# Kernel tuning notes

Hardware: AMD Instinct MI355X
Metric: run time of the kernel (lower is better)

## Reference

```python
import jax, jax.numpy as jnp
import numpy as np

TEMP = 0.1
DX = 64  # feature dim of x; W1 rows [0:DX] multiply x, rows [DX:] multiply y


def setup_inputs() -> dict:
    key = jax.random.key(0)
    k1, k2, k3, k4 = jax.random.split(key, 4)
    n, d, hidden = 1024, 64, 256
    x = jax.random.normal(k1, (n, d), dtype=jnp.float32)
    y = jax.random.normal(k2, (n, d), dtype=jnp.float32)
    W1 = jax.random.normal(k3, (2 * d, hidden), dtype=jnp.float32) * (1.0 / np.sqrt(2 * d))
    b1 = jnp.zeros((hidden,), dtype=jnp.float32)
    w2 = jax.random.normal(k4, (hidden,), dtype=jnp.float32) * (1.0 / np.sqrt(hidden))
    b2 = jnp.zeros((), dtype=jnp.float32)
    return {"x": x, "y": y, "W1": W1, "b1": b1, "w2": w2, "b2": b2}


def reference(x, y, W1, b1, w2, b2):
    n = y.shape[0]
    W1x, W1y = W1[:DX], W1[DX:]
    xp = x @ W1x                      # [n, hidden], indexed by j (x_tile[i,j] = x[j])
    yp = y @ W1y                      # [n, hidden], indexed by i (y_tile[i,j] = y[i])
    # Positive pairs: scorer(cat(x_i, y_i))
    pos = (jax.nn.relu(xp + yp + b1) @ w2 + b2) / TEMP          # [n]
    h = jax.nn.relu(yp[:, None, :] + xp[None, :, :] + b1)        # [n, n, hidden]
    scores = (h @ w2 + b2) / TEMP                                 # [n, n]
    lse = jax.nn.logsumexp(scores, axis=1)                        # [n]
    lower_bound = pos.mean() - (lse.mean() - jnp.log(jnp.float32(n)))
    return -lower_bound
```

## Files before the change

kernel.cpp:

```cpp
#include <hip/hip_runtime.h>
#include <math.h>

#define NN 1024
#define DD 64
#define HH 256
#define TEMP_INV 10.0f
#define KCH 64
#define NCH 4

typedef float v2f __attribute__((ext_vector_type(2)));


__global__ __launch_bounds__(256)
void k1_proj(const float* __restrict__ x, const float* __restrict__ y,
             const float* __restrict__ W1, const float* __restrict__ b1,
             float* __restrict__ x2T, float* __restrict__ y2)
{
    const int tid = threadIdx.x;
    const int i0 = blockIdx.x * 2;
    float ax0 = 0.f, ax1 = 0.f, ay0 = 0.f, ay1 = 0.f;
    #pragma unroll 8
    for (int kk = 0; kk < DD; ++kk) {
        const float wx = W1[kk * HH + tid];
        const float wy = W1[(DD + kk) * HH + tid];
        ax0 = fmaf(x[i0 * DD + kk],       wx, ax0);
        ax1 = fmaf(x[(i0 + 1) * DD + kk], wx, ax1);
        ay0 = fmaf(y[i0 * DD + kk],       wy, ay0);
        ay1 = fmaf(y[(i0 + 1) * DD + kk], wy, ay1);
    }
    const float b1t = b1[tid];
    *(float2*)&x2T[tid * NN + i0] = make_float2(ax0 + b1t, ax1 + b1t);
    y2[i0 * HH + tid]       = ay0;
    y2[(i0 + 1) * HH + tid] = ay1;
}

__global__ __launch_bounds__(256, 2)
void k2_scores(const float* __restrict__ x2T, const float* __restrict__ y2,
               const float* __restrict__ w2, const float* __restrict__ b2,
               float* __restrict__ pmax, float* __restrict__ psum,
               float* __restrict__ pos)
{
    __shared__ float xs[2][KCH][64];
    const int t  = threadIdx.x;
    const int bj = blockIdx.x;
    const int bi = blockIdx.y;
    const int j0 = bj * 64;
    const int rr = t >> 5;
    const int cc = t & 31;
    const int rbase = bi * 32 + rr * 4;
    const float* yb = y2 + rbase * HH;

    const int wv  = t >> 6;
    const int ln  = t & 63;
    const int sro = ln >> 4;
    const int sco = (ln & 15) * 4;

    v2f acc[4];
    #pragma unroll
    for (int p = 0; p < 4; ++p) acc[p] = (v2f){0.f, 0.f};
    const v2f zero = {0.f, 0.f};

    #define STAGE(c, b)                                                        \
    {                                                                          \
        _Pragma("unroll")                                                      \
        for (int h = 0; h < 4; ++h) {                                          \
            const int row = wv * 16 + h * 4;                                   \
            const float* gsrc =                                               \
                &x2T[((c) * KCH + row + sro) * NN + j0 + sco];                 \
            __builtin_amdgcn_global_load_lds(                                  \
                (const __attribute__((address_space(1))) unsigned int*)gsrc,   \
                (__attribute__((address_space(3))) unsigned int*)&xs[b][row][0],\
                16, 0, 0);                                                     \
        }                                                                      \
    }

    STAGE(0, 0);
    for (int c = 0; c < NCH; ++c) {
        __syncthreads();
        if (c + 1 < NCH) STAGE(c + 1, (c + 1) & 1);
        const int cur = c & 1;
        #pragma unroll
        for (int g = 0; g < 16; ++g) {
            const int gg = c * 16 + g;
            float4 yv4[4];
            #pragma unroll
            for (int p = 0; p < 4; ++p)
                yv4[p] = *(const float4*)&yb[p * HH + gg * 4];
            #pragma unroll
            for (int e = 0; e < 4; ++e) {
                const float wk = w2[gg * 4 + e];
                const v2f wv2 = {wk, wk};
                const v2f xv = *(const v2f*)&xs[cur][g * 4 + e][cc * 2];
                #pragma unroll
                for (int p = 0; p < 4; ++p) {
                    const float yv = (e == 0) ? yv4[p].x : (e == 1) ? yv4[p].y
                                   : (e == 2) ? yv4[p].z : yv4[p].w;
                    v2f z = xv + (v2f){yv, yv};
                    z = __builtin_elementwise_max(z, zero);
                    acc[p] = z * wv2 + acc[p];
                }
            }
        }
    }
    #undef STAGE

    const float bb = b2[0];
    const v2f bbv = {bb, bb};
    v2f sc[4];
    #pragma unroll
    for (int p = 0; p < 4; ++p) sc[p] = (acc[p] + bbv) * TEMP_INV;

    const int col0 = j0 + cc * 2;
    #pragma unroll
    for (int p = 0; p < 4; ++p) {
        const int row = rbase + p;
        if (row == col0)     pos[row] = sc[p].x;
        if (row == col0 + 1) pos[row] = sc[p].y;
    }

    float m[4], e[4];
    #pragma unroll
    for (int p = 0; p < 4; ++p) {
        m[p] = fmaxf(sc[p].x, sc[p].y);
        e[p] = __expf(sc[p].x - m[p]) + __expf(sc[p].y - m[p]);
    }
    #pragma unroll
    for (int mk = 16; mk >= 1; mk >>= 1) {
        #pragma unroll
        for (int p = 0; p < 4; ++p) {
            const float mo = __shfl_xor(m[p], mk);
            const float eo = __shfl_xor(e[p], mk);
            const float mn = fmaxf(m[p], mo);
            e[p] = e[p] * __expf(m[p] - mn) + eo * __expf(mo - mn);
            m[p] = mn;
        }
    }
    if (cc == 0) {
        #pragma unroll
        for (int p = 0; p < 4; ++p) {
            pmax[bj * NN + rbase + p] = m[p];
            psum[bj * NN + rbase + p] = e[p];
        }
    }
}

__global__ __launch_bounds__(1024)
void k3_final(const float* __restrict__ pmax, const float* __restrict__ psum,
              const float* __restrict__ pos, float* __restrict__ out)
{
    __shared__ float2 red[1024];
    const int tid = threadIdx.x;
    float M = pmax[tid], E = psum[tid];
    #pragma unroll
    for (int jc = 1; jc < 16; ++jc) {
        const float Mo = pmax[jc * NN + tid];
        const float Eo = psum[jc * NN + tid];
        const float Mn = fmaxf(M, Mo);
        E = E * __expf(M - Mn) + Eo * __expf(Mo - Mn);
        M = Mn;
    }
    red[tid] = make_float2(M + logf(E), pos[tid]);
    __syncthreads();
    for (int s = 512; s > 0; s >>= 1) {
        if (tid < s) {
            const float2 o = red[tid + s];
            float2 m2 = red[tid];
            m2.x += o.x; m2.y += o.y;
            red[tid] = m2;
        }
        __syncthreads();
    }
    if (tid == 0)
        out[0] = red[0].x / (float)NN - logf((float)NN) - red[0].y / (float)NN;
}

extern "C" void kernel_launch(void* const* d_in, const int* in_sizes, int n_in,
                              void* d_out, int out_size, void* d_ws, size_t ws_size,
                              hipStream_t stream)
{
    const float* x  = (const float*)d_in[0];
    const float* y  = (const float*)d_in[1];
    const float* W1 = (const float*)d_in[2];
    const float* b1 = (const float*)d_in[3];
    const float* w2 = (const float*)d_in[4];
    const float* b2 = (const float*)d_in[5];
    float* out = (float*)d_out;

    float* ws   = (float*)d_ws;
    float* x2T  = ws;
    float* y2   = x2T + HH * NN;
    float* pmax = y2 + NN * HH;
    float* psum = pmax + 16 * NN;
    float* pos  = psum + 16 * NN;

    hipLaunchKernelGGL(k1_proj, dim3(NN / 2), dim3(256), 0, stream,
                       x, y, W1, b1, x2T, y2);
    hipLaunchKernelGGL(k2_scores, dim3(16, 32), dim3(256), 0, stream,
                       x2T, y2, w2, b2, pmax, psum, pos);
    hipLaunchKernelGGL(k3_final, dim3(1), dim3(1024), 0, stream,
                       pmax, psum, pos, out);
}
```

Baseline: 40.74 us.

## Fold w2 into projections and sort hidden units by sign of w2

The projection kernel now scales the x and y projections by w2. It reorders hidden units so that those with non-negative w2 come first, and records their count. The score kernel then uses relu(a)*w = max(aw,0) for w>=0 and min(aw,0) for w<0, which drops the multiply from the inner loop and leaves only an add. The positive-pair scores are now computed and reduced in the projection kernel instead of on the diagonal of the score kernel. This adds a block reduction and a ballot/prefix step in k1, plus branchy sign-boundary handling in the inner loop.

After: 45.96 us. 1.13x slower.

```diff
diff --git a/kernel.cpp b/kernel.cpp
--- a/kernel.cpp
+++ b/kernel.cpp
@@ -14,8 +14,12 @@
 __global__ __launch_bounds__(256)
 void k1_proj(const float* __restrict__ x, const float* __restrict__ y,
              const float* __restrict__ W1, const float* __restrict__ b1,
-             float* __restrict__ x2T, float* __restrict__ y2)
-{
+             const float* __restrict__ w2,
+             float* __restrict__ x2T, float* __restrict__ y2,
+             float* __restrict__ posr, int* __restrict__ kposD)
+{
+    __shared__ float red[2][256];
+    __shared__ unsigned int cnts[4];
     const int tid = threadIdx.x;
     const int i0 = blockIdx.x * 2;
     float ax0 = 0.f, ax1 = 0.f, ay0 = 0.f, ay1 = 0.f;
@@ -28,17 +32,44 @@
         ay0 = fmaf(y[i0 * DD + kk],       wy, ay0);
         ay1 = fmaf(y[(i0 + 1) * DD + kk], wy, ay1);
     }
-    const float b1t = b1[tid];
-    *(float2*)&x2T[tid * NN + i0] = make_float2(ax0 + b1t, ax1 + b1t);
-    y2[i0 * HH + tid]       = ay0;
-    y2[(i0 + 1) * HH + tid] = ay1;
+    const float w2t = w2[tid], b1t = b1[tid];
+    const float xb0 = ax0 + b1t, xb1 = ax1 + b1t;
+    const float p0 = fmaxf(ay0 + xb0, 0.f) * w2t;
+    const float p1 = fmaxf(ay1 + xb1, 0.f) * w2t;
+
+    const int lane = tid & 63, wv = tid >> 6;
+    const bool nonneg = (w2t >= 0.f);
+    const unsigned long long bal = __ballot(nonneg);
+    const int before = __popcll(bal & ((1ull << lane) - 1ull));
+    if (lane == 0) cnts[wv] = (unsigned int)__popcll(bal);
+    __syncthreads();
+    const int kpos = (int)(cnts[0] + cnts[1] + cnts[2] + cnts[3]);
+    int posbase = 0;
+    for (int u = 0; u < wv; ++u) posbase += (int)cnts[u];
+    const int rank = nonneg ? (posbase + before)
+                            : (kpos + wv * 64 - posbase + lane - before);
+
+    *(float2*)&x2T[rank * NN + i0] = make_float2(xb0 * w2t, xb1 * w2t);
+    y2[i0 * HH + rank]       = ay0 * w2t;
+    y2[(i0 + 1) * HH + rank] = ay1 * w2t;
+    if (blockIdx.x == 0 && tid == 0) kposD[0] = kpos;
+
+    red[0][tid] = p0; red[1][tid] = p1;
+    __syncthreads();
+    for (int s = 128; s > 0; s >>= 1) {
+        if (tid < s) {
+            red[0][tid] += red[0][tid + s];
+            red[1][tid] += red[1][tid + s];
+        }
+        __syncthreads();
+    }
+    if (tid == 0) { posr[i0] = red[0][0]; posr[i0 + 1] = red[1][0]; }
 }
 
 __global__ __launch_bounds__(256, 2)
 void k2_scores(const float* __restrict__ x2T, const float* __restrict__ y2,
-               const float* __restrict__ w2, const float* __restrict__ b2,
-               float* __restrict__ pmax, float* __restrict__ psum,
-               float* __restrict__ pos)
+               const float* __restrict__ b2, const int* __restrict__ kposD,
+               float* __restrict__ pmax, float* __restrict__ psum)
 {
     __shared__ float xs[2][KCH][64];
     const int t  = threadIdx.x;
@@ -49,6 +80,7 @@
     const int cc = t & 31;
     const int rbase = bi * 32 + rr * 4;
     const float* yb = y2 + rbase * HH;
+    const int kpos = kposD[0];
 
     const int wv  = t >> 6;
     const int ln  = t & 63;
@@ -74,35 +106,52 @@
         }                                                                      \
     }
 
+    #define BODY(OPMAX, KL, YV)                                                \
+    {                                                                          \
+        const v2f xv = *(const v2f*)&xs[cur][KL][cc * 2];                      \
+        _Pragma("unroll")                                                      \
+        for (int p = 0; p < 4; ++p) {                                          \
+            const float yv = (YV);                                             \
+            v2f z = xv + (v2f){yv, yv};                                        \
+            z = OPMAX ? __builtin_elementwise_max(z, zero)                     \
+                      : __builtin_elementwise_min(z, zero);                    \
+            acc[p] = acc[p] + z;                                               \
+        }                                                                      \
+    }
+    #define YE(e) ((e == 0) ? yv4[p].x : (e == 1) ? yv4[p].y                   \
+                 : (e == 2) ? yv4[p].z : yv4[p].w)
+
     STAGE(0, 0);
     for (int c = 0; c < NCH; ++c) {
         __syncthreads();
         if (c + 1 < NCH) STAGE(c + 1, (c + 1) & 1);
         const int cur = c & 1;
+        const int m = kpos - c * KCH;
         #pragma unroll
         for (int g = 0; g < 16; ++g) {
-            const int gg = c * 16 + g;
+            const int kb = g * 4;
             float4 yv4[4];
             #pragma unroll
             for (int p = 0; p < 4; ++p)
-                yv4[p] = *(const float4*)&yb[p * HH + gg * 4];
-            #pragma unroll
-            for (int e = 0; e < 4; ++e) {
-                const float wk = w2[gg * 4 + e];
-                const v2f wv2 = {wk, wk};
-                const v2f xv = *(const v2f*)&xs[cur][g * 4 + e][cc * 2];
+                yv4[p] = *(const float4*)&yb[p * HH + c * KCH + kb];
+            if (kb + 4 <= m) {
                 #pragma unroll
-                for (int p = 0; p < 4; ++p) {
-                    const float yv = (e == 0) ? yv4[p].x : (e == 1) ? yv4[p].y
-                                   : (e == 2) ? yv4[p].z : yv4[p].w;
-                    v2f z = xv + (v2f){yv, yv};
-                    z = __builtin_elementwise_max(z, zero);
-                    acc[p] = z * wv2 + acc[p];
+                for (int e = 0; e < 4; ++e) BODY(1, kb + e, YE(e));
+            } else if (kb >= m) {
+                #pragma unroll
+                for (int e = 0; e < 4; ++e) BODY(0, kb + e, YE(e));
+            } else {
+                #pragma unroll
+                for (int e = 0; e < 4; ++e) {
+                    if (kb + e < m) BODY(1, kb + e, YE(e))
+                    else            BODY(0, kb + e, YE(e));
                 }
             }
         }
     }
     #undef STAGE
+    #undef BODY
+    #undef YE
 
     const float bb = b2[0];
     const v2f bbv = {bb, bb};
@@ -110,46 +159,40 @@
     #pragma unroll
     for (int p = 0; p < 4; ++p) sc[p] = (acc[p] + bbv) * TEMP_INV;
 
-    const int col0 = j0 + cc * 2;
+    float m_[4], e_[4];
     #pragma unroll
     for (int p = 0; p < 4; ++p) {
-        const int row = rbase + p;
-        if (row == col0)     pos[row] = sc[p].x;
-        if (row == col0 + 1) pos[row] = sc[p].y;
-    }
-
-    float m[4], e[4];
-    #pragma unroll
-    for (int p = 0; p < 4; ++p) {
-        m[p] = fmaxf(sc[p].x, sc[p].y);
-        e[p] = __expf(sc[p].x - m[p]) + __expf(sc[p].y - m[p]);
+        m_[p] = fmaxf(sc[p].x, sc[p].y);
+        e_[p] = __expf(sc[p].x - m_[p]) + __expf(sc[p].y - m_[p]);
     }
     #pragma unroll
     for (int mk = 16; mk >= 1; mk >>= 1) {
         #pragma unroll
         for (int p = 0; p < 4; ++p) {
-            const float mo = __shfl_xor(m[p], mk);
-            const float eo = __shfl_xor(e[p], mk);
-            const float mn = fmaxf(m[p], mo);
-            e[p] = e[p] * __expf(m[p] - mn) + eo * __expf(mo - mn);
-            m[p] = mn;
+            const float mo = __shfl_xor(m_[p], mk);
+            const float eo = __shfl_xor(e_[p], mk);
+            const float mn = fmaxf(m_[p], mo);
+            e_[p] = e_[p] * __expf(m_[p] - mn) + eo * __expf(mo - mn);
+            m_[p] = mn;
         }
     }
     if (cc == 0) {
         #pragma unroll
         for (int p = 0; p < 4; ++p) {
-            pmax[bj * NN + rbase + p] = m[p];
-            psum[bj * NN + rbase + p] = e[p];
+            pmax[bj * NN + rbase + p] = m_[p];
+            psum[bj * NN + rbase + p] = e_[p];
         }
     }
 }
 
 __global__ __launch_bounds__(1024)
 void k3_final(const float* __restrict__ pmax, const float* __restrict__ psum,
-              const float* __restrict__ pos, float* __restrict__ out)
+              const float* __restrict__ posr, const float* __restrict__ b2,
+              float* __restrict__ out)
 {
     __shared__ float2 red[1024];
     const int tid = threadIdx.x;
+    const float bb = b2[0];
     float M = pmax[tid], E = psum[tid];
     #pragma unroll
     for (int jc = 1; jc < 16; ++jc) {
@@ -159,7 +202,7 @@
         E = E * __expf(M - Mn) + Eo * __expf(Mo - Mn);
         M = Mn;
     }
-    red[tid] = make_float2(M + logf(E), pos[tid]);
+    red[tid] = make_float2(M + logf(E), (posr[tid] + bb) * TEMP_INV);
     __syncthreads();
     for (int s = 512; s > 0; s >>= 1) {
         if (tid < s) {
@@ -191,12 +234,13 @@
     float* y2   = x2T + HH * NN;
     float* pmax = y2 + NN * HH;
     float* psum = pmax + 16 * NN;
-    float* pos  = psum + 16 * NN;
+    float* posr = psum + 16 * NN;
+    int*  kposD = (int*)(posr + NN);
 
     hipLaunchKernelGGL(k1_proj, dim3(NN / 2), dim3(256), 0, stream,
-                       x, y, W1, b1, x2T, y2);
+                       x, y, W1, b1, w2, x2T, y2, posr, kposD);
     hipLaunchKernelGGL(k2_scores, dim3(16, 32), dim3(256), 0, stream,
-                       x2T, y2, w2, b2, pmax, psum, pos);
+                       x2T, y2, b2, kposD, pmax, psum);
     hipLaunchKernelGGL(k3_final, dim3(1), dim3(1024), 0, stream,
-                       pmax, psum, pos, out);
-}
+                       pmax, psum, posr, b2, out);
+}
```

## Fuse final reduction into score kernel via atomics and last-block ticket

Applied to the files above, without the earlier changes.

Removes the separate single-block final kernel. Row-wise exp sums and the positive-pair sum are now accumulated with global atomics, and the last block to finish, chosen by an atomic ticket counter, computes the log-sum and writes the output. The numerically safe running-max logsumexp is replaced by raw exp sums without max subtraction, which relies on scores staying small enough not to overflow. The intent is to save one kernel launch and the partial-buffer traffic, at the cost of atomic contention and order-dependent rounding.

After: 41.02 us. About the same (+0.7%).

```diff
diff --git a/kernel.cpp b/kernel.cpp
--- a/kernel.cpp
+++ b/kernel.cpp
@@ -7,6 +7,7 @@
 #define TEMP_INV 10.0f
 #define KCH 64
 #define NCH 4
+#define NBLK2 512u
 
 typedef float v2f __attribute__((ext_vector_type(2)));
 
@@ -14,9 +15,15 @@
 __global__ __launch_bounds__(256)
 void k1_proj(const float* __restrict__ x, const float* __restrict__ y,
              const float* __restrict__ W1, const float* __restrict__ b1,
-             float* __restrict__ x2T, float* __restrict__ y2)
+             float* __restrict__ x2T, float* __restrict__ y2,
+             float* __restrict__ E, float* __restrict__ gacc,
+             unsigned int* __restrict__ tick)
 {
     const int tid = threadIdx.x;
+    if (blockIdx.x == 0) {
+        *(float4*)&E[tid * 4] = make_float4(0.f, 0.f, 0.f, 0.f);
+        if (tid == 0) { gacc[0] = 0.f; gacc[1] = 0.f; tick[0] = 0u; }
+    }
     const int i0 = blockIdx.x * 2;
     float ax0 = 0.f, ax1 = 0.f, ay0 = 0.f, ay1 = 0.f;
     #pragma unroll 8
@@ -37,10 +44,12 @@
 __global__ __launch_bounds__(256, 2)
 void k2_scores(const float* __restrict__ x2T, const float* __restrict__ y2,
                const float* __restrict__ w2, const float* __restrict__ b2,
-               float* __restrict__ pmax, float* __restrict__ psum,
-               float* __restrict__ pos)
+               float* __restrict__ E, float* __restrict__ gacc,
+               unsigned int* __restrict__ tick, float* __restrict__ out)
 {
     __shared__ float xs[2][KCH][64];
+    __shared__ float redf[256];
+    __shared__ unsigned int s_old;
     const int t  = threadIdx.x;
     const int bj = blockIdx.x;
     const int bi = blockIdx.y;
@@ -111,67 +120,57 @@
     for (int p = 0; p < 4; ++p) sc[p] = (acc[p] + bbv) * TEMP_INV;
 
     const int col0 = j0 + cc * 2;
+    float dv = 0.f; bool isd = false;
     #pragma unroll
     for (int p = 0; p < 4; ++p) {
         const int row = rbase + p;
-        if (row == col0)     pos[row] = sc[p].x;
-        if (row == col0 + 1) pos[row] = sc[p].y;
+        if (row == col0)     { dv += sc[p].x; isd = true; }
+        if (row == col0 + 1) { dv += sc[p].y; isd = true; }
     }
+    if (isd) atomicAdd(&gacc[1], dv);
 
-    float m[4], e[4];
+    float e_[4];
     #pragma unroll
-    for (int p = 0; p < 4; ++p) {
-        m[p] = fmaxf(sc[p].x, sc[p].y);
-        e[p] = __expf(sc[p].x - m[p]) + __expf(sc[p].y - m[p]);
-    }
+    for (int p = 0; p < 4; ++p)
+        e_[p] = __expf(sc[p].x) + __expf(sc[p].y);
     #pragma unroll
     for (int mk = 16; mk >= 1; mk >>= 1) {
         #pragma unroll
-        for (int p = 0; p < 4; ++p) {
-            const float mo = __shfl_xor(m[p], mk);
-            const float eo = __shfl_xor(e[p], mk);
-            const float mn = fmaxf(m[p], mo);
-            e[p] = e[p] * __expf(m[p] - mn) + eo * __expf(mo - mn);
-            m[p] = mn;
-        }
+        for (int p = 0; p < 4; ++p)
+            e_[p] += __shfl_xor(e_[p], mk);
     }
     if (cc == 0) {
         #pragma unroll
-        for (int p = 0; p < 4; ++p) {
-            pmax[bj * NN + rbase + p] = m[p];
-            psum[bj * NN + rbase + p] = e[p];
+        for (int p = 0; p < 4; ++p)
+            atomicAdd(&E[rbase + p], e_[p]);
+    }
+
+    asm volatile("s_waitcnt vmcnt(0)" ::: "memory");
+    __syncthreads();
+    if (t == 0) s_old = atomicAdd(tick, 1u);
+    __syncthreads();
+    if (s_old == NBLK2 - 1u) {
+        float ls = 0.f;
+        #pragma unroll
+        for (int r = 0; r < 4; ++r) {
+            const float ev = __hip_atomic_load(&E[t + r * 256],
+                                               __ATOMIC_RELAXED,
+                                               __HIP_MEMORY_SCOPE_AGENT);
+            ls += logf(ev);
+        }
+        redf[t] = ls;
+        __syncthreads();
+        for (int s2 = 128; s2 > 0; s2 >>= 1) {
+            if (t < s2) redf[t] += redf[t + s2];
+            __syncthreads();
+        }
+        if (t == 0) {
+            const float pos_sum = __hip_atomic_load(&gacc[1], __ATOMIC_RELAXED,
+                                                    __HIP_MEMORY_SCOPE_AGENT);
+            out[0] = redf[0] / (float)NN - logf((float)NN)
+                   - pos_sum / (float)NN;
         }
     }
-}
-
-__global__ __launch_bounds__(1024)
-void k3_final(const float* __restrict__ pmax, const float* __restrict__ psum,
-              const float* __restrict__ pos, float* __restrict__ out)
-{
-    __shared__ float2 red[1024];
-    const int tid = threadIdx.x;
-    float M = pmax[tid], E = psum[tid];
-    #pragma unroll
-    for (int jc = 1; jc < 16; ++jc) {
-        const float Mo = pmax[jc * NN + tid];
-        const float Eo = psum[jc * NN + tid];
-        const float Mn = fmaxf(M, Mo);
-        E = E * __expf(M - Mn) + Eo * __expf(Mo - Mn);
-        M = Mn;
-    }
-    red[tid] = make_float2(M + logf(E), pos[tid]);
-    __syncthreads();
-    for (int s = 512; s > 0; s >>= 1) {
-        if (tid < s) {
-            const float2 o = red[tid + s];
-            float2 m2 = red[tid];
-            m2.x += o.x; m2.y += o.y;
-            red[tid] = m2;
-        }
-        __syncthreads();
-    }
-    if (tid == 0)
-        out[0] = red[0].x / (float)NN - logf((float)NN) - red[0].y / (float)NN;
 }
 
 extern "C" void kernel_launch(void* const* d_in, const int* in_sizes, int n_in,
@@ -189,14 +188,12 @@
     float* ws   = (float*)d_ws;
     float* x2T  = ws;
     float* y2   = x2T + HH * NN;
-    float* pmax = y2 + NN * HH;
-    float* psum = pmax + 16 * NN;
-    float* pos  = psum + 16 * NN;
+    float* E    = y2 + NN * HH;
+    float* gacc = E + NN;
+    unsigned int* tick = (unsigned int*)(gacc + 2);
 
     hipLaunchKernelGGL(k1_proj, dim3(NN / 2), dim3(256), 0, stream,
-                       x, y, W1, b1, x2T, y2);
+                       x, y, W1, b1, x2T, y2, E, gacc, tick);
     hipLaunchKernelGGL(k2_scores, dim3(16, 32), dim3(256), 0, stream,
-                       x2T, y2, w2, b2, pmax, psum, pos);
-    hipLaunchKernelGGL(k3_final, dim3(1), dim3(1024), 0, stream,
-                       pmax, psum, pos, out);
+                       x2T, y2, w2, b2, E, gacc, tick, out);
 }
```
